# Kernel tuning notes

Measured on AMD Instinct MI355X. Metric: run time of the kernel, lower is better.

The kernel has to match this reference:

```python
import jax, jax.numpy as jnp
import numpy as np

B, S, IN, E, L = 8, 1024, 768, 256, 12

def setup_inputs() -> dict:
    key = jax.random.key(0)
    k1, k2, k3, k4 = jax.random.split(key, 4)
    input_tensor = jax.random.normal(k1, (B, S, IN), dtype=jnp.float32)
    fc_w = jax.random.normal(k2, (E, IN), dtype=jnp.float32) * (1.0 / np.sqrt(IN))
    fc_b = jax.random.normal(k3, (E,), dtype=jnp.float32) * 0.02
    bi_w = jax.random.normal(k4, (E * L, E), dtype=jnp.float32) * (1.0 / np.sqrt(E))
    bias = jnp.zeros((E,), dtype=jnp.float32)
    return {"input_tensor": input_tensor, "fc_w": fc_w, "fc_b": fc_b, "bi_w": bi_w, "bias": bias}

def reference(input_tensor, fc_w, fc_b, bi_w, bias):
    # fc: [B,S,IN] -> [B,S,E]
    t = jnp.einsum('bsi,ei->bse', input_tensor, fc_w) + fc_b
    # bi_linear: [B,S,E] -> [B,S,L,E], plus bias over E
    bl = jnp.einsum('bse,fe->bsf', t, bi_w).reshape(B, S, L, E) + bias
    # bilinear score: out[b,i,l,j] = sum_e bl[b,i,l,e] * t[b,j,e]
    # (avoids materializing the O(B*S*S*E) expanded value tensor)
    return jnp.einsum('bile,bje->bilj', bl, t)
```

## Files before the change

kernel.cpp:

```cpp
#include <hip/hip_runtime.h>
#include <hip/hip_bf16.h>

typedef __bf16 bf16_t;
typedef __bf16 bf16x8 __attribute__((ext_vector_type(8)));
typedef __bf16 bf16x4 __attribute__((ext_vector_type(4)));
typedef float f32x4 __attribute__((ext_vector_type(4)));

__global__ __launch_bounds__(256)
void cvt_all(const float* __restrict__ in, bf16_t* __restrict__ o_in,
             const float* __restrict__ fw, bf16_t* __restrict__ o_fw,
             const float* __restrict__ bw, bf16_t* __restrict__ o_bw) {
    int i = blockIdx.x * 256 + threadIdx.x;
    const float* s;
    bf16_t* d;
    int k;
    if (i < 786432)      { s = in; d = o_in; k = i; }
    else if (i < 811008) { s = fw; d = o_fw; k = i - 786432; }
    else if (i < 909312) { s = bw; d = o_bw; k = i - 811008; }
    else return;
    float4 a = ((const float4*)s)[k * 2];
    float4 b = ((const float4*)s)[k * 2 + 1];
    bf16x8 v;
    v[0] = (bf16_t)a.x; v[1] = (bf16_t)a.y; v[2] = (bf16_t)a.z; v[3] = (bf16_t)a.w;
    v[4] = (bf16_t)b.x; v[5] = (bf16_t)b.y; v[6] = (bf16_t)b.z; v[7] = (bf16_t)b.w;
    ((bf16x8*)d)[k] = v;
}

template <int BM, int BN, int EPI>
__global__ __launch_bounds__(256)
void gemm_bt(const bf16_t* __restrict__ A, const bf16_t* __restrict__ Bm,
             void* __restrict__ Cv, const float* __restrict__ bias,
             int M, int N, int K) {
    constexpr int MR = BM / 32;
    constexpr int NR = BN / 32;
    typedef float fvec __attribute__((ext_vector_type(NR)));
    typedef bf16_t bvec __attribute__((ext_vector_type(NR)));

    __shared__ bf16_t As[BM * 64];
    __shared__ bf16_t Bs[BN * 64];

    const int tid  = threadIdx.x;
    const int lane = tid & 63;
    const int wave = tid >> 6;
    const int mblk = blockIdx.x, nblk = blockIdx.y;

    const bf16_t* Ab = A + (long)mblk * BM * K;
    const bf16_t* Bb = Bm + (long)nblk * BN * K;

    f32x4 acc[MR][NR] = {};

    const int wrow = (wave >> 1) * (BM / 2);
    const int wcol = (wave & 1) * (BN / 2);
    const int lrow = lane & 15;
    const int kgrp = lane >> 4;

    for (int k0 = 0; k0 < K; k0 += 64) {
#pragma unroll
        for (int it = 0; it < MR; ++it) {
            const int chunk = it * 256 + tid;
            const int row = chunk >> 3, c8 = chunk & 7;
            __builtin_amdgcn_global_load_lds(
                (const __attribute__((address_space(1))) void*)(Ab + (long)row * K + k0 + c8 * 8),
                (__attribute__((address_space(3))) void*)(As + chunk * 8), 16, 0, 0);
        }
#pragma unroll
        for (int it = 0; it < NR; ++it) {
            const int chunk = it * 256 + tid;
            const int row = chunk >> 3, c8 = chunk & 7;
            __builtin_amdgcn_global_load_lds(
                (const __attribute__((address_space(1))) void*)(Bb + (long)row * K + k0 + c8 * 8),
                (__attribute__((address_space(3))) void*)(Bs + chunk * 8), 16, 0, 0);
        }
        __syncthreads();

#pragma unroll
        for (int kk = 0; kk < 64; kk += 32) {
            const int koff = kk + kgrp * 8;
            bf16x8 af[MR], bfr[NR];
#pragma unroll
            for (int m = 0; m < MR; ++m)
                af[m] = *(const bf16x8*)(As + (wrow + m * 16 + lrow) * 64 + koff);
#pragma unroll
            for (int n = 0; n < NR; ++n)
                bfr[n] = *(const bf16x8*)(Bs + (wcol + lrow * NR + n) * 64 + koff);
#pragma unroll
            for (int m = 0; m < MR; ++m)
#pragma unroll
                for (int n = 0; n < NR; ++n)
                    acc[m][n] = __builtin_amdgcn_mfma_f32_16x16x32_bf16(af[m], bfr[n], acc[m][n], 0, 0, 0);
        }
        __syncthreads();
    }

    const long rbase = (long)mblk * BM + wrow + kgrp * 4;
    const long cb0   = (long)nblk * BN + wcol + lrow * NR;
    bf16_t* C = (bf16_t*)Cv;
    const float* bp = bias + cb0;
    fvec bv = *(const fvec*)bp;
#pragma unroll
    for (int m = 0; m < MR; ++m)
#pragma unroll
        for (int j = 0; j < 4; ++j) {
            bvec v;
#pragma unroll
            for (int n = 0; n < NR; ++n) v[n] = (bf16_t)(acc[m][n][j] + bv[n]);
            *(bvec*)(C + (rbase + m * 16 + j) * N + cb0) = v;
        }
}

template <int EPI, int XCD, int NMB, int NNB>
__global__ __launch_bounds__(512, 2)
void gemm8p(const bf16_t* __restrict__ A, const bf16_t* __restrict__ Bm,
            void* __restrict__ Cv, const float* __restrict__ bias,
            int N, long sA, long sB, long sC) {
    constexpr int K = 256;
    extern __shared__ bf16_t lds[];

    const int tid  = threadIdx.x;
    const int lane = tid & 63;
    const int wave = tid >> 6;
    const int wm = wave >> 2, wn = wave & 3;
    const int lrow = lane & 15, kgrp = lane >> 4;

    int mblk, nblk, bz;
    {
        int L = blockIdx.x;
        if (XCD) { bz = L & 7; int w = L >> 3; nblk = w % NNB; mblk = w / NNB; }
        else     { bz = 0;     mblk = L % NMB; nblk = L / NMB; }
    }

    const bf16_t* Ab = A + (long)bz * sA + (long)mblk * 256 * K;
    const bf16_t* Bb = Bm + (long)bz * sB + (long)nblk * 256 * K;

    const int c0 = tid, c1 = 512 + tid;
    const int r0 = c0 >> 3, r1 = c1 >> 3;
    const int ca0 = (c0 & 7) ^ (r0 & 7),        ca1 = (c1 & 7) ^ (r1 & 7);
    const int cb0 = (c0 & 7) ^ ((r0 >> 2) & 7), cb1 = (c1 & 7) ^ ((r1 >> 2) & 7);

    auto stageA = [&](int t, int h) {
        const bf16_t* s0 = Ab + (long)(h * 128 + r0) * K + t * 64 + ca0 * 8;
        const bf16_t* s1 = Ab + (long)(h * 128 + r1) * K + t * 64 + ca1 * 8;
        bf16_t* d = lds + ((t & 1) * 2 + h) * 8192;
        __builtin_amdgcn_global_load_lds((const __attribute__((address_space(1))) void*)s0,
            (__attribute__((address_space(3))) void*)(d + c0 * 8), 16, 0, 0);
        __builtin_amdgcn_global_load_lds((const __attribute__((address_space(1))) void*)s1,
            (__attribute__((address_space(3))) void*)(d + c1 * 8), 16, 0, 0);
    };
    auto stageB = [&](int t, int h) {
        const bf16_t* s0 = Bb + (long)(h * 128 + r0) * K + t * 64 + cb0 * 8;
        const bf16_t* s1 = Bb + (long)(h * 128 + r1) * K + t * 64 + cb1 * 8;
        bf16_t* d = lds + 32768 + ((t & 1) * 2 + h) * 8192;
        __builtin_amdgcn_global_load_lds((const __attribute__((address_space(1))) void*)s0,
            (__attribute__((address_space(3))) void*)(d + c0 * 8), 16, 0, 0);
        __builtin_amdgcn_global_load_lds((const __attribute__((address_space(1))) void*)s1,
            (__attribute__((address_space(3))) void*)(d + c1 * 8), 16, 0, 0);
    };
    auto ldA = [&](int t, int mf, int kk) -> bf16x8 {
        const int row = mf * 16 + lrow;
        const int col = (kk * 32 + kgrp * 8) ^ ((row & 7) << 3);
        return *(const bf16x8*)(lds + ((t & 1) * 2 + wm) * 8192 + row * 64 + col);
    };
    auto ldB = [&](int t, int g, int kk) -> bf16x8 {
        const int row = (wn & 1) * 64 + lrow * 4 + g;
        const int col = (kk * 32 + kgrp * 8) ^ (((row >> 2) & 7) << 3);
        return *(const bf16x8*)(lds + 32768 + ((t & 1) * 2 + (wn >> 1)) * 8192 + row * 64 + col);
    };

    f32x4 acc[8][4] = {};
    bf16x8 bfr[4][2];

    stageA(0, 0); stageA(0, 1); stageB(0, 0); stageB(0, 1); stageB(1, 0); stageB(1, 1);
    asm volatile("s_waitcnt vmcnt(4)" ::: "memory");
    __builtin_amdgcn_s_barrier();

#pragma unroll
    for (int i = 0; i < 2; ++i) {
#pragma unroll
        for (int p = 0; p < 8; ++p) {
            const int q = p & 3;
            const int t = 2 * i + (p >> 2);
            bf16x8 af[2][2];
            if (q == 0) {
#pragma unroll
                for (int g = 0; g < 4; ++g) { bfr[g][0] = ldB(t, g, 0); bfr[g][1] = ldB(t, g, 1); }
            }
#pragma unroll
            for (int mm = 0; mm < 2; ++mm) { af[mm][0] = ldA(t, 2 * q + mm, 0); af[mm][1] = ldA(t, 2 * q + mm, 1); }

            if (p == 0) stageA(2 * i + 1, 0);
            else if (p == 1) stageA(2 * i + 1, 1);
            else if (p == 2) { if (2 * i + 2 < 4) stageB(2 * i + 2, 0); }
            else if (p == 3) { if (2 * i + 2 < 4) stageB(2 * i + 2, 1); }
            else if (p == 4) { if (2 * i + 2 < 4) stageA(2 * i + 2, 0); }
            else if (p == 5) { if (2 * i + 2 < 4) stageA(2 * i + 2, 1); }
            else if (p == 6) { if (2 * i + 3 < 4) stageB(2 * i + 3, 0); }
            else             { if (2 * i + 3 < 4) stageB(2 * i + 3, 1); }

            __builtin_amdgcn_s_barrier();
            asm volatile("s_waitcnt lgkmcnt(0)" ::: "memory");
            __builtin_amdgcn_s_setprio(1);
#pragma unroll
            for (int mm = 0; mm < 2; ++mm)
#pragma unroll
                for (int g = 0; g < 4; ++g)
#pragma unroll
                    for (int kk = 0; kk < 2; ++kk)
                        acc[2 * q + mm][g] = __builtin_amdgcn_mfma_f32_16x16x32_bf16(
                            af[mm][kk], bfr[g][kk], acc[2 * q + mm][g], 0, 0, 0);
            __builtin_amdgcn_s_setprio(0);

            if (p == 3) {
                if (2 * i + 2 < 4) asm volatile("s_waitcnt vmcnt(4)" ::: "memory");
                else               asm volatile("s_waitcnt vmcnt(0)" ::: "memory");
            } else if (p == 7) {
                if (2 * i + 2 < 4) asm volatile("s_waitcnt vmcnt(4)" ::: "memory");
            }
            __builtin_amdgcn_s_barrier();
        }
    }

    const long rb = (long)mblk * 256 + wm * 128 + kgrp * 4;
    const long cb = (long)nblk * 256 + wn * 64 + lrow * 4;
    if constexpr (EPI == 0) {
        float* C = (float*)Cv + (long)bz * sC;
#pragma unroll
        for (int m = 0; m < 8; ++m)
#pragma unroll
            for (int j = 0; j < 4; ++j) {
                f32x4 v = { acc[m][0][j], acc[m][1][j], acc[m][2][j], acc[m][3][j] };
                __builtin_nontemporal_store(v, (f32x4*)(C + (rb + m * 16 + j) * N + cb));
            }
    } else {
        bf16_t* C = (bf16_t*)Cv;
        f32x4 bv = *(const f32x4*)(bias + (int)(cb & 255));
#pragma unroll
        for (int m = 0; m < 8; ++m)
#pragma unroll
            for (int j = 0; j < 4; ++j) {
                bf16x4 v;
#pragma unroll
                for (int g = 0; g < 4; ++g) v[g] = (bf16_t)(acc[m][g][j] + bv[g]);
                *(bf16x4*)(C + (rb + m * 16 + j) * N + cb) = v;
            }
    }
}

extern "C" void kernel_launch(void* const* d_in, const int* in_sizes, int n_in,
                              void* d_out, int out_size, void* d_ws, size_t ws_size,
                              hipStream_t stream) {
    const float* input = (const float*)d_in[0];
    const float* fc_w  = (const float*)d_in[1];
    const float* fc_b  = (const float*)d_in[2];
    const float* bi_w  = (const float*)d_in[3];
    const float* bias  = (const float*)d_in[4];

    char* ws = (char*)d_ws;
    bf16_t* inA = (bf16_t*)(ws);
    bf16_t* wfc = (bf16_t*)(ws + 12582912);
    bf16_t* wbi = (bf16_t*)(ws + 12976128);
    bf16_t* t   = (bf16_t*)(ws + 14548992);
    bf16_t* bl  = (bf16_t*)(ws + 18743296);

    cvt_all<<<dim3(3552), dim3(256), 0, stream>>>(input, inA, fc_w, wfc, bi_w, wbi);

    gemm_bt<64, 64, 1><<<dim3(128, 4), dim3(256), 0, stream>>>(
        inA, wfc, (void*)t, fc_b, 8192, 256, 768);

    gemm8p<2, 0, 32, 12><<<dim3(384), dim3(512), 131072, stream>>>(
        t, wbi, (void*)bl, bias, 3072, 0L, 0L, 0L);

    gemm8p<0, 1, 48, 4><<<dim3(1536), dim3(512), 131072, stream>>>(
        bl, t, d_out, nullptr, 1024,
        (long)12288 * 256, (long)1024 * 256, (long)12288 * 1024);
}
```

Measured before the change: 135.9 us.

## Replace final batched GEMM with dedicated 192x128-tile K=256 kernel

Adds a specialized kernel for the last bilinear GEMM (K fixed at 256). It uses 192x128 tiles with 256 threads and two blocks per CU, double-buffered direct global-to-LDS loads with XOR swizzle, and s_setprio around the MFMA block. The aim is better occupancy and latency hiding for this output-write-bound stage than the generic 8-wave kernel gives. In exchange it hardcodes the shapes (N=1024, K=256, batch=8) and uses a smaller tile, so operand reuse per block is lower.

```diff
diff --git a/kernel.cpp b/kernel.cpp
--- a/kernel.cpp
+++ b/kernel.cpp
@@ -245,6 +245,98 @@
     }
 }
 
+template <int NNB>
+__global__ __launch_bounds__(256, 2)
+void gemm3k(const bf16_t* __restrict__ A, const bf16_t* __restrict__ Bm,
+            float* __restrict__ C, long sA, long sB, long sC) {
+    constexpr int K = 256, BM = 192, BN = 128;
+    extern __shared__ bf16_t lds[];
+
+    const int tid  = threadIdx.x;
+    const int lane = tid & 63;
+    const int wave = tid >> 6;
+    const int wm = wave >> 1, wn = wave & 1;
+    const int lrow = lane & 15, kgrp = lane >> 4;
+
+    const int L = blockIdx.x;
+    const int bz = L & 7;
+    const int w = L >> 3;
+    const int nblk = w & (NNB - 1), mblk = w / NNB;
+
+    const bf16_t* Ab = A + (long)bz * sA + (long)mblk * BM * K;
+    const bf16_t* Bb = Bm + (long)bz * sB + (long)nblk * BN * K;
+
+    auto stage = [&](int t) {
+        const int buf = t & 1;
+#pragma unroll
+        for (int it = 0; it < 6; ++it) {
+            const int c = it * 256 + tid, row = c >> 3;
+            const int sa = (c & 7) ^ (row & 7);
+            __builtin_amdgcn_global_load_lds(
+                (const __attribute__((address_space(1))) void*)(Ab + (long)row * K + t * 64 + sa * 8),
+                (__attribute__((address_space(3))) void*)(lds + buf * 12288 + c * 8), 16, 0, 0);
+        }
+#pragma unroll
+        for (int it = 0; it < 4; ++it) {
+            const int c = it * 256 + tid, row = c >> 3;
+            const int sb = (c & 7) ^ ((row >> 2) & 7);
+            __builtin_amdgcn_global_load_lds(
+                (const __attribute__((address_space(1))) void*)(Bb + (long)row * K + t * 64 + sb * 8),
+                (__attribute__((address_space(3))) void*)(lds + 24576 + buf * 8192 + c * 8), 16, 0, 0);
+        }
+    };
+
+    f32x4 acc[6][4] = {};
+
+    stage(0);
+    __syncthreads();
+
+#pragma unroll
+    for (int t = 0; t < 4; ++t) {
+        if (t < 3) stage(t + 1);
+        const int buf = t & 1;
+        bf16x8 af[6][2], bfr[4][2];
+#pragma unroll
+        for (int m = 0; m < 6; ++m) {
+            const int r = wm * 96 + m * 16 + lrow;
+#pragma unroll
+            for (int kk = 0; kk < 2; ++kk)
+                af[m][kk] = *(const bf16x8*)(lds + buf * 12288 + r * 64 +
+                                             ((kk * 32 + kgrp * 8) ^ ((r & 7) << 3)));
+        }
+#pragma unroll
+        for (int g = 0; g < 4; ++g) {
+            const int r = wn * 64 + lrow * 4 + g;
+#pragma unroll
+            for (int kk = 0; kk < 2; ++kk)
+                bfr[g][kk] = *(const bf16x8*)(lds + 24576 + buf * 8192 + r * 64 +
+                                              ((kk * 32 + kgrp * 8) ^ (((r >> 2) & 7) << 3)));
+        }
+        __builtin_amdgcn_s_setprio(1);
+#pragma unroll
+        for (int m = 0; m < 6; ++m)
+#pragma unroll
+            for (int g = 0; g < 4; ++g)
+#pragma unroll
+                for (int kk = 0; kk < 2; ++kk)
+                    acc[m][g] = __builtin_amdgcn_mfma_f32_16x16x32_bf16(
+                        af[m][kk], bfr[g][kk], acc[m][g], 0, 0, 0);
+        __builtin_amdgcn_s_setprio(0);
+        __syncthreads();
+    }
+
+    float* Cb = C + (long)bz * sC;
+    const long rb = (long)mblk * BM + wm * 96 + kgrp * 4;
+    const long cb = (long)nblk * BN + wn * 64 + lrow * 4;
+#pragma unroll
+    for (int m = 0; m < 6; ++m)
+#pragma unroll
+        for (int j = 0; j < 4; ++j) {
+            f32x4 v = { acc[m][0][j], acc[m][1][j], acc[m][2][j], acc[m][3][j] };
+            __builtin_nontemporal_store(v, (f32x4*)(Cb + (rb + m * 16 + j) * 1024 + cb));
+        }
+}
+
 extern "C" void kernel_launch(void* const* d_in, const int* in_sizes, int n_in,
                               void* d_out, int out_size, void* d_ws, size_t ws_size,
                               hipStream_t stream) {
@@ -269,7 +361,7 @@
     gemm8p<2, 0, 32, 12><<<dim3(384), dim3(512), 131072, stream>>>(
         t, wbi, (void*)bl, bias, 3072, 0L, 0L, 0L);
 
-    gemm8p<0, 1, 48, 4><<<dim3(1536), dim3(512), 131072, stream>>>(
-        bl, t, d_out, nullptr, 1024,
+    gemm3k<8><<<dim3(4096), dim3(256), 81920, stream>>>(
+        bl, t, (float*)d_out,
         (long)12288 * 256, (long)1024 * 256, (long)12288 * 1024);
 }
```

After: 125.0 us. 8.1% less time.
